# Performance work log

Hardware: AMD Instinct MI355X
Metric: run time of the kernel (lower is better)

## Reference

```python
import jax, jax.numpy as jnp
import numpy as np

N_NODES = 200000
N_EDGES = 4000000
NUM_BASIS = 10
MAX_RADIUS = 1.0
NUM_NEIGHBORS = 10
HIDDEN = 16
# e3nn FCTP(0e+1o+2e, 0e+1o+2e -> 0e): 3 paths (l x l -> 0e), path coeff = 1/sqrt(n_paths*(2l+1))
PATH_C = np.array([1.0 / np.sqrt(3.0 * (2 * l + 1)) for l in (0, 1, 2)], dtype=np.float32)


def _spherical_harmonics_l2(v):
    """e3nn spherical harmonics lmax=2, normalize=True, 'component' normalization. v: [E,3] -> [E,9]."""
    r = jnp.linalg.norm(v, axis=-1, keepdims=True)
    u = v / jnp.maximum(r, 1e-12)
    x, y, z = u[:, 0], u[:, 1], u[:, 2]
    s3, s5 = np.sqrt(3.0).astype(np.float32), np.sqrt(5.0).astype(np.float32)
    sh0 = jnp.ones_like(x)[:, None]                      # [E,1]
    sh1 = s3 * u                                         # [E,3]
    x2, y2, z2 = x * x, y * y, z * z
    sh2 = s5 * jnp.stack([s3 * x * z,
                          s3 * x * y,
                          y2 - 0.5 * (x2 + z2),
                          s3 * y * z,
                          0.5 * s3 * (z2 - x2)], axis=-1)  # [E,5]
    return jnp.concatenate([sh0, sh1, sh2], axis=-1)


def _radial_embedding(r):
    """e3nn soft_one_hot_linspace(basis='smooth_finite', cutoff=True) * sqrt(num_basis). r: [E] -> [E,NUM_BASIS]."""
    values = jnp.linspace(0.0, MAX_RADIUS, NUM_BASIS + 2)[1:-1]
    step = MAX_RADIUS / (NUM_BASIS + 1)
    diff = (r[:, None] - values) / step

    def soft_unit_step(t):
        return jnp.where(t > 0, jnp.exp(-1.0 / jnp.where(t > 0, t, 1.0)), 0.0)

    y = np.float32(1.14136 * np.exp(2.0)) * soft_unit_step(diff + 1.0) * soft_unit_step(1.0 - diff)
    return y * np.float32(np.sqrt(NUM_BASIS))


def setup_inputs() -> dict:
    key = jax.random.key(0)
    k1, k2, k3, k4, k5, k6 = jax.random.split(key, 6)
    node_feats = jax.random.normal(k1, (N_NODES, 9), dtype=jnp.float32)
    edge_vec = 0.25 * jax.random.normal(k2, (N_EDGES, 3), dtype=jnp.float32)  # keep norms mostly < max_radius
    edge_src = jax.random.randint(k3, (N_EDGES,), 0, N_NODES)
    edge_dst = jax.random.randint(k4, (N_EDGES,), 0, N_NODES)
    W1 = jax.random.normal(k5, (NUM_BASIS, HIDDEN), dtype=jnp.float32)
    W2 = jax.random.normal(k6, (HIDDEN, 3), dtype=jnp.float32)
    return {"node_feats": node_feats, "edge_vec": edge_vec, "W1": W1, "W2": W2,
            "edge_src": edge_src, "edge_dst": edge_dst}


def reference(node_feats, edge_vec, W1, W2, edge_src, edge_dst):
    r = jnp.linalg.norm(edge_vec, axis=-1)                      # [E]
    sh = _spherical_harmonics_l2(edge_vec)                      # [E,9]
    emb = _radial_embedding(r)                                  # [E,NUM_BASIS]
    # e3nn FullyConnectedNet([num_basis, 16, 3], relu): variance-preserving layers
    h = np.float32(np.sqrt(2.0)) * jax.nn.relu(emb @ W1 / np.float32(np.sqrt(NUM_BASIS)))
    w = h @ W2 / np.float32(np.sqrt(HIDDEN))                    # [E,3] per-edge TP weights
    f = node_feats[edge_src]                                    # gather [E,9]
    # FCTP paths: l x l -> 0e reduces to per-l dot products
    dots = jnp.stack([f[:, 0] * sh[:, 0],
                      jnp.sum(f[:, 1:4] * sh[:, 1:4], axis=-1),
                      jnp.sum(f[:, 4:9] * sh[:, 4:9], axis=-1)], axis=-1)  # [E,3]
    edge_out = jnp.sum(w * jnp.asarray(PATH_C) * dots, axis=-1)            # [E]
    node_out = jax.ops.segment_sum(edge_out, edge_dst, num_segments=N_NODES)
    node_out = node_out / np.float32(np.sqrt(NUM_NEIGHBORS))
    return node_out.sum()
```

## Files before the change

### kernel.cpp

```cpp
#include <hip/hip_runtime.h>
#include <hip/hip_fp16.h>

#define NTHREADS 256
#define NBLOCKS 2048
#define FB_NBLOCKS 2048
#define NB 1024
#define NBP 1040

#define KTOT 11.9269705f
#define CL0  0.04564355f
#define CL1  0.02635231f
#define CL2  0.02041241f
#define S3   1.7320508f
#define S5   2.2360680f

__device__ __forceinline__ float fast_rcp(float x) { return __builtin_amdgcn_rcpf(x); }

__global__ __launch_bounds__(256) void pack_feats_14(
    const float* __restrict__ nf, uint4* __restrict__ tab, int n_nodes)
{
    const int n = blockIdx.x * 256 + threadIdx.x;
    if (n >= n_nodes) return;
    const float* f = nf + 9 * (size_t)n;
    const float scale[9] = { 1.0f, S3, S3, S3, S5 * S3, S5 * S3, S5, S5 * S3,
                             0.5f * S5 * S3 };
    unsigned short hs[9];
#pragma unroll
    for (int i = 0; i < 9; ++i) {
        const __half h = __float2half_rn(f[i] * scale[i]);
        hs[i] = *reinterpret_cast<const unsigned short*>(&h);
    }
    unsigned long long c[9];
#pragma unroll
    for (int i = 1; i < 9; ++i)
        c[i] = (unsigned long long)(((unsigned)hs[i] + 2u) >> 2) & 0x3FFFull;
    const unsigned long long lo =
        c[1] | (c[2] << 14) | (c[3] << 28) | (c[4] << 42) | (c[5] << 56);
    const unsigned long long hi =
        (c[5] >> 8) | (c[6] << 6) | (c[7] << 20) | (c[8] << 34) |
        ((unsigned long long)hs[0] << 48);
    tab[n] = make_uint4((unsigned)lo, (unsigned)(lo >> 32),
                        (unsigned)hi, (unsigned)(hi >> 32));
}

__global__ __launch_bounds__(256) void build_wtable_kernel(
    const float* __restrict__ W1, const float* __restrict__ W2,
    float* __restrict__ wtab)
{
    const int idx = blockIdx.x * 256 + threadIdx.x;
    if (idx > NB) return;
    const float r = (float)idx * (1.0f / (float)NB);

    const float t    = 11.0f * r;
    const int   k0   = (int)t;
    const float frac = t - (float)k0;
    float ea = 0.0f, eb = 0.0f;
    if (k0 >= 1 && k0 <= 10) {
        const float da = fmaf(-frac, frac, 1.0f);
        if (da > 0.0226f) ea = KTOT * __expf(-2.0f * fast_rcp(da));
    }
    if (k0 <= 9) {
        const float db = frac * (2.0f - frac);
        if (db > 0.0226f) eb = KTOT * __expf(-2.0f * fast_rcp(db));
    }
    const int ra = min(max(k0 - 1, 0), 9);
    const int rb = min(k0, 9);

    float w0 = 0.0f, w1 = 0.0f, w2 = 0.0f;
#pragma unroll
    for (int j = 0; j < 16; ++j) {
        const float h = fmaxf(fmaf(ea, W1[ra * 16 + j], eb * W1[rb * 16 + j]), 0.0f);
        w0 = fmaf(h, W2[j * 3 + 0], w0);
        w1 = fmaf(h, W2[j * 3 + 1], w1);
        w2 = fmaf(h, W2[j * 3 + 2], w2);
    }
    wtab[idx]           = w0 * CL0;
    wtab[NBP + idx]     = w1 * CL1;
    wtab[2 * NBP + idx] = w2 * CL2;
}

__device__ __forceinline__ float cvt14(unsigned c) {
    __half_raw hr; hr.x = (unsigned short)(c << 2);
    return __half2float(*reinterpret_cast<const __half*>(&hr));
}
__device__ __forceinline__ float cvt16(unsigned c) {
    __half_raw hr; hr.x = (unsigned short)c;
    return __half2float(*reinterpret_cast<const __half*>(&hr));
}
__device__ __forceinline__ unsigned alignb(unsigned hi, unsigned lo, int s) {
    return (lo >> s) | (hi << (32 - s));
}

__device__ __forceinline__ float edge_term_lut(
    float vx, float vy, float vz, uint4 g,
    const float* __restrict__ sw)
{
    const float r2 = fmaf(vx, vx, fmaf(vy, vy, vz * vz));
    const float rs = rsqrtf(fmaxf(r2, 1e-24f));
    const float r  = r2 * rs;
    const float x = vx * rs, y = vy * rs, z = vz * rs;

    const float tb = fminf(r, 1.0f) * (float)NB;
    const int   i  = min((int)tb, NB - 1);
    const float fb = tb - (float)i;
    const float w0a = sw[i],           w0b = sw[i + 1];
    const float w1a = sw[NBP + i],     w1b = sw[NBP + i + 1];
    const float w2a = sw[2 * NBP + i], w2b = sw[2 * NBP + i + 1];
    const float wv0 = fmaf(fb, w0b - w0a, w0a);
    const float wv1 = fmaf(fb, w1b - w1a, w1a);
    const float wv2 = fmaf(fb, w2b - w2a, w2a);

    const float fv1 = cvt14(g.x & 0x3FFFu);
    const float fv2 = cvt14((g.x >> 14) & 0x3FFFu);
    const float fv3 = cvt14(alignb(g.y, g.x, 28) & 0x3FFFu);
    const float fv4 = cvt14((g.y >> 10) & 0x3FFFu);
    const float fv5 = cvt14(alignb(g.z, g.y, 24) & 0x3FFFu);
    const float fv6 = cvt14((g.z >> 6) & 0x3FFFu);
    const float fv7 = cvt14(alignb(g.w, g.z, 20) & 0x3FFFu);
    const float fv8 = cvt14((g.w >> 2) & 0x3FFFu);
    const float f0  = cvt16(g.w >> 16);

    const float dots0 = f0;
    const float dots1 = fmaf(fv1, x, fmaf(fv2, y, fv3 * z));
    const float xx = x * x, yy = y * y, zz = z * z;
    const float dots2 = fmaf(fv4, x * z, fmaf(fv5, x * y,
                        fmaf(fv6, fmaf(-0.5f, xx + zz, yy),
                        fmaf(fv7, y * z, fv8 * (zz - xx)))));

    return fmaf(wv0, dots0, fmaf(wv1, dots1, wv2 * dots2));
}

__global__ __launch_bounds__(NTHREADS) void edge_sum_p14(
    const float4* __restrict__ ev4,
    const int4*   __restrict__ src4,
    const uint4*  __restrict__ tab,
    const float*  __restrict__ wtab,
    float*        __restrict__ block_sums,
    int n_edges)
{
    __shared__ float sw[3 * NBP];
    const int tid = threadIdx.x;
    for (int i = tid; i < 3 * NBP; i += NTHREADS) sw[i] = wtab[i];
    __syncthreads();

    float acc = 0.0f;
    const int n_groups = (n_edges + 3) >> 2;
    const int stride = gridDim.x * blockDim.x;
    for (int g = blockIdx.x * blockDim.x + tid; g < n_groups; g += stride) {
        const int e0 = g << 2;
        if (e0 + 3 < n_edges) {
            const float4 a = ev4[3 * (size_t)g + 0];
            const float4 b = ev4[3 * (size_t)g + 1];
            const float4 c = ev4[3 * (size_t)g + 2];
            const int4   s = src4[g];
            const uint4 g0 = tab[s.x];
            const uint4 g1 = tab[s.y];
            const uint4 g2 = tab[s.z];
            const uint4 g3 = tab[s.w];
            acc += edge_term_lut(a.x, a.y, a.z, g0, sw);
            acc += edge_term_lut(a.w, b.x, b.y, g1, sw);
            acc += edge_term_lut(b.z, b.w, c.x, g2, sw);
            acc += edge_term_lut(c.y, c.z, c.w, g3, sw);
        } else {
            const float* evf  = reinterpret_cast<const float*>(ev4);
            const int*   srci = reinterpret_cast<const int*>(src4);
            for (int e = e0; e < n_edges; ++e) {
                acc += edge_term_lut(evf[3 * (size_t)e], evf[3 * (size_t)e + 1],
                                     evf[3 * (size_t)e + 2], tab[srci[e]], sw);
            }
        }
    }

#pragma unroll
    for (int off = 1; off < 64; off <<= 1)
        acc += __shfl_xor(acc, off, 64);
    __shared__ float wsum[NTHREADS / 64];
    const int lane = tid & 63, wid = tid >> 6;
    if (lane == 0) wsum[wid] = acc;
    __syncthreads();
    if (tid == 0) {
        float ssum = 0.0f;
#pragma unroll
        for (int w = 0; w < NTHREADS / 64; ++w) ssum += wsum[w];
        block_sums[blockIdx.x] = ssum;
    }
}

__global__ __launch_bounds__(NTHREADS) void edge_sum_fallback(
    const float* __restrict__ node_feats,
    const float* __restrict__ edge_vec,
    const float* __restrict__ W1,
    const float* __restrict__ W2,
    const int*   __restrict__ edge_src,
    float*       __restrict__ block_sums,
    int n_edges)
{
    __shared__ float4 sW1[10][5];
    float* sW1f = reinterpret_cast<float*>(sW1);
    const int tid = threadIdx.x;
    if (tid < 160) {
        sW1f[(tid >> 4) * 20 + (tid & 15)] = W1[tid];
    } else if (tid < 200) {
        const int i = tid - 160;
        sW1f[(i >> 2) * 20 + 16 + (i & 3)] = 0.0f;
    }
    __syncthreads();

    float w2r[16][3];
#pragma unroll
    for (int j = 0; j < 16; ++j) {
        w2r[j][0] = W2[j * 3 + 0] * CL0;
        w2r[j][1] = W2[j * 3 + 1] * CL1;
        w2r[j][2] = W2[j * 3 + 2] * CL2;
    }

    float acc = 0.0f;
    const int stride = gridDim.x * blockDim.x;
    for (int e = blockIdx.x * blockDim.x + tid; e < n_edges; e += stride) {
        const float vx = edge_vec[3 * (size_t)e + 0];
        const float vy = edge_vec[3 * (size_t)e + 1];
        const float vz = edge_vec[3 * (size_t)e + 2];
        const int   src = edge_src[e];
        const float* f = node_feats + 9 * (size_t)src;
        const float r2 = fmaf(vx, vx, fmaf(vy, vy, vz * vz));
        const float rs = rsqrtf(fmaxf(r2, 1e-24f));
        const float r  = r2 * rs;
        const float x = vx * rs, y = vy * rs, z = vz * rs;
        const float t    = 11.0f * r;
        const int   k0   = (int)t;
        const float frac = t - (float)k0;
        float ea = 0.0f, eb = 0.0f;
        if (k0 >= 1 && k0 <= 10) {
            const float da = fmaf(-frac, frac, 1.0f);
            if (da > 0.0226f) ea = KTOT * __expf(-2.0f * fast_rcp(da));
        }
        if (k0 <= 9) {
            const float db = frac * (2.0f - frac);
            if (db > 0.0226f) eb = KTOT * __expf(-2.0f * fast_rcp(db));
        }
        const int ra = min(max(k0 - 1, 0), 9);
        const int rb = min(k0, 9);
        const float4* rowA = &sW1[ra][0];
        const float4* rowB = &sW1[rb][0];
        float wv0 = 0.0f, wv1 = 0.0f, wv2 = 0.0f;
#pragma unroll
        for (int q = 0; q < 4; ++q) {
            const float4 A = rowA[q];
            const float4 B = rowB[q];
            float h;
            h = fmaxf(fmaf(ea, A.x, eb * B.x), 0.0f);
            wv0 = fmaf(h, w2r[4 * q + 0][0], wv0); wv1 = fmaf(h, w2r[4 * q + 0][1], wv1); wv2 = fmaf(h, w2r[4 * q + 0][2], wv2);
            h = fmaxf(fmaf(ea, A.y, eb * B.y), 0.0f);
            wv0 = fmaf(h, w2r[4 * q + 1][0], wv0); wv1 = fmaf(h, w2r[4 * q + 1][1], wv1); wv2 = fmaf(h, w2r[4 * q + 1][2], wv2);
            h = fmaxf(fmaf(ea, A.z, eb * B.z), 0.0f);
            wv0 = fmaf(h, w2r[4 * q + 2][0], wv0); wv1 = fmaf(h, w2r[4 * q + 2][1], wv1); wv2 = fmaf(h, w2r[4 * q + 2][2], wv2);
            h = fmaxf(fmaf(ea, A.w, eb * B.w), 0.0f);
            wv0 = fmaf(h, w2r[4 * q + 3][0], wv0); wv1 = fmaf(h, w2r[4 * q + 3][1], wv1); wv2 = fmaf(h, w2r[4 * q + 3][2], wv2);
        }
        const float f0 = f[0], f1 = f[1], f2 = f[2], f3 = f[3], f4 = f[4];
        const float f5 = f[5], f6 = f[6], f7 = f[7], f8 = f[8];
        const float dots0 = f0;
        const float dots1 = S3 * fmaf(f1, x, fmaf(f2, y, f3 * z));
        const float xx = x * x, yy = y * y, zz = z * z;
        const float sh20 = S5 * S3 * x * z;
        const float sh21 = S5 * S3 * x * y;
        const float sh22 = S5 * (yy - 0.5f * (xx + zz));
        const float sh23 = S5 * S3 * y * z;
        const float sh24 = S5 * 0.5f * S3 * (zz - xx);
        const float dots2 = fmaf(f4, sh20, fmaf(f5, sh21, fmaf(f6, sh22, fmaf(f7, sh23, f8 * sh24))));
        acc = fmaf(wv0, dots0, acc);
        acc = fmaf(wv1, dots1, acc);
        acc = fmaf(wv2, dots2, acc);
    }
#pragma unroll
    for (int off = 1; off < 64; off <<= 1)
        acc += __shfl_xor(acc, off, 64);
    __shared__ float wsum[NTHREADS / 64];
    const int lane = tid & 63, wid = tid >> 6;
    if (lane == 0) wsum[wid] = acc;
    __syncthreads();
    if (tid == 0) {
        float ssum = 0.0f;
#pragma unroll
        for (int w = 0; w < NTHREADS / 64; ++w) ssum += wsum[w];
        block_sums[blockIdx.x] = ssum;
    }
}

__global__ __launch_bounds__(256) void final_reduce_kernel(
    const float* __restrict__ block_sums, float* __restrict__ out, int n)
{
    const int tid = threadIdx.x;
    float acc = 0.0f;
    for (int i = tid; i < n; i += 256) acc += block_sums[i];
#pragma unroll
    for (int off = 1; off < 64; off <<= 1)
        acc += __shfl_xor(acc, off, 64);
    __shared__ float wsum[4];
    if ((tid & 63) == 0) wsum[tid >> 6] = acc;
    __syncthreads();
    if (tid == 0) out[0] = wsum[0] + wsum[1] + wsum[2] + wsum[3];
}

extern "C" void kernel_launch(void* const* d_in, const int* in_sizes, int n_in,
                              void* d_out, int out_size, void* d_ws, size_t ws_size,
                              hipStream_t stream) {
    const float* node_feats = (const float*)d_in[0];
    const float* edge_vec   = (const float*)d_in[1];
    const float* W1         = (const float*)d_in[2];
    const float* W2         = (const float*)d_in[3];
    const int*   edge_src   = (const int*)d_in[4];
    const int n_edges = in_sizes[4];
    const int n_nodes = in_sizes[0] / 9;

    float* block_sums = (float*)d_ws;
    const size_t wtab_off = 32768;
    const size_t tab_off  = wtab_off + ((3 * NBP * 4 + 255) & ~255);
    const size_t need     = tab_off + (size_t)n_nodes * 16;

    if (ws_size >= need) {
        float* wtab = (float*)((char*)d_ws + wtab_off);
        uint4* tab  = (uint4*)((char*)d_ws + tab_off);
        pack_feats_14<<<(n_nodes + 255) / 256, 256, 0, stream>>>(
            node_feats, tab, n_nodes);
        build_wtable_kernel<<<(NB + 256) / 256, 256, 0, stream>>>(W1, W2, wtab);
        edge_sum_p14<<<NBLOCKS, NTHREADS, 0, stream>>>(
            (const float4*)edge_vec, (const int4*)edge_src, tab,
            wtab, block_sums, n_edges);
        final_reduce_kernel<<<1, 256, 0, stream>>>(block_sums, (float*)d_out, NBLOCKS);
    } else {
        edge_sum_fallback<<<FB_NBLOCKS, NTHREADS, 0, stream>>>(
            node_feats, edge_vec, W1, W2, edge_src, block_sums, n_edges);
        final_reduce_kernel<<<1, 256, 0, stream>>>(block_sums, (float*)d_out, FB_NBLOCKS);
    }
}
```

Before: 46.79 us.

## Pack radial weight LUT into fp16 base+delta records and process 8 edges per thread

Replaces the three separate float LUT arrays with a single 16-byte record per bin holding fp16 bases and slopes, so each edge does one LDS vector read instead of six scalar reads. Each thread now handles 8 edges per iteration with more outstanding gathers, and the grid is halved. An extra small kernel builds the packed table; fp16 weights reduce precision of the interpolation.

```diff
diff --git a/kernel.cpp b/kernel.cpp
--- a/kernel.cpp
+++ b/kernel.cpp
@@ -2,7 +2,7 @@
 #include <hip/hip_fp16.h>
 
 #define NTHREADS 256
-#define NBLOCKS 2048
+#define NBLOCKS 1024
 #define FB_NBLOCKS 2048
 #define NB 1024
 #define NBP 1040
@@ -45,7 +45,7 @@
 
 __global__ __launch_bounds__(256) void build_wtable_kernel(
     const float* __restrict__ W1, const float* __restrict__ W2,
-    float* __restrict__ wtab)
+    float* __restrict__ wtabf)
 {
     const int idx = blockIdx.x * 256 + threadIdx.x;
     if (idx > NB) return;
@@ -74,9 +74,26 @@
         w1 = fmaf(h, W2[j * 3 + 1], w1);
         w2 = fmaf(h, W2[j * 3 + 2], w2);
     }
-    wtab[idx]           = w0 * CL0;
-    wtab[NBP + idx]     = w1 * CL1;
-    wtab[2 * NBP + idx] = w2 * CL2;
+    wtabf[idx]           = w0 * CL0;
+    wtabf[NBP + idx]     = w1 * CL1;
+    wtabf[2 * NBP + idx] = w2 * CL2;
+}
+
+__global__ __launch_bounds__(256) void build_wrec_kernel(
+    const float* __restrict__ wtabf, uint4* __restrict__ wrec)
+{
+    const int i = blockIdx.x * 256 + threadIdx.x;
+    if (i >= NB) return;
+    const float w0a = wtabf[i],           w0b = wtabf[i + 1];
+    const float w1a = wtabf[NBP + i],     w1b = wtabf[NBP + i + 1];
+    const float w2a = wtabf[2 * NBP + i], w2b = wtabf[2 * NBP + i + 1];
+    auto hbits = [](float v) -> unsigned {
+        const __half h = __float2half_rn(v);
+        return (unsigned)*reinterpret_cast<const unsigned short*>(&h);
+    };
+    const unsigned b0 = hbits(w0a), b1 = hbits(w1a), b2 = hbits(w2a);
+    const unsigned d0 = hbits(w0b - w0a), d1 = hbits(w1b - w1a), d2 = hbits(w2b - w2a);
+    wrec[i] = make_uint4(b0 | (b1 << 16), b2 | (d0 << 16), d1 | (d2 << 16), 0u);
 }
 
 __device__ __forceinline__ float cvt14(unsigned c) {
@@ -84,16 +101,15 @@
     return __half2float(*reinterpret_cast<const __half*>(&hr));
 }
 __device__ __forceinline__ float cvt16(unsigned c) {
-    __half_raw hr; hr.x = (unsigned short)c;
+    __half_raw hr; hr.x = (unsigned short)(c & 0xFFFFu);
     return __half2float(*reinterpret_cast<const __half*>(&hr));
 }
 __device__ __forceinline__ unsigned alignb(unsigned hi, unsigned lo, int s) {
     return (lo >> s) | (hi << (32 - s));
 }
 
-__device__ __forceinline__ float edge_term_lut(
-    float vx, float vy, float vz, uint4 g,
-    const float* __restrict__ sw)
+__device__ __forceinline__ float edge_term(
+    float vx, float vy, float vz, uint4 g, const uint4* __restrict__ swq)
 {
     const float r2 = fmaf(vx, vx, fmaf(vy, vy, vz * vz));
     const float rs = rsqrtf(fmaxf(r2, 1e-24f));
@@ -103,12 +119,10 @@
     const float tb = fminf(r, 1.0f) * (float)NB;
     const int   i  = min((int)tb, NB - 1);
     const float fb = tb - (float)i;
-    const float w0a = sw[i],           w0b = sw[i + 1];
-    const float w1a = sw[NBP + i],     w1b = sw[NBP + i + 1];
-    const float w2a = sw[2 * NBP + i], w2b = sw[2 * NBP + i + 1];
-    const float wv0 = fmaf(fb, w0b - w0a, w0a);
-    const float wv1 = fmaf(fb, w1b - w1a, w1a);
-    const float wv2 = fmaf(fb, w2b - w2a, w2a);
+    const uint4 q = swq[i];
+    const float wv0 = fmaf(fb, cvt16(q.y >> 16), cvt16(q.x));
+    const float wv1 = fmaf(fb, cvt16(q.z),       cvt16(q.x >> 16));
+    const float wv2 = fmaf(fb, cvt16(q.z >> 16), cvt16(q.y));
 
     const float fv1 = cvt14(g.x & 0x3FFFu);
     const float fv2 = cvt14((g.x >> 14) & 0x3FFFu);
@@ -130,43 +144,56 @@
     return fmaf(wv0, dots0, fmaf(wv1, dots1, wv2 * dots2));
 }
 
-__global__ __launch_bounds__(NTHREADS) void edge_sum_p14(
+__global__ __launch_bounds__(NTHREADS) void edge_sum_p14w(
     const float4* __restrict__ ev4,
     const int4*   __restrict__ src4,
     const uint4*  __restrict__ tab,
-    const float*  __restrict__ wtab,
+    const uint4*  __restrict__ wrec,
     float*        __restrict__ block_sums,
     int n_edges)
 {
-    __shared__ float sw[3 * NBP];
+    __shared__ uint4 swq[NB];
     const int tid = threadIdx.x;
-    for (int i = tid; i < 3 * NBP; i += NTHREADS) sw[i] = wtab[i];
+#pragma unroll
+    for (int i = tid; i < NB; i += NTHREADS) swq[i] = wrec[i];
     __syncthreads();
 
     float acc = 0.0f;
-    const int n_groups = (n_edges + 3) >> 2;
+    const int n_units = (n_edges + 7) >> 3;
     const int stride = gridDim.x * blockDim.x;
-    for (int g = blockIdx.x * blockDim.x + tid; g < n_groups; g += stride) {
-        const int e0 = g << 2;
-        if (e0 + 3 < n_edges) {
-            const float4 a = ev4[3 * (size_t)g + 0];
-            const float4 b = ev4[3 * (size_t)g + 1];
-            const float4 c = ev4[3 * (size_t)g + 2];
-            const int4   s = src4[g];
-            const uint4 g0 = tab[s.x];
-            const uint4 g1 = tab[s.y];
-            const uint4 g2 = tab[s.z];
-            const uint4 g3 = tab[s.w];
-            acc += edge_term_lut(a.x, a.y, a.z, g0, sw);
-            acc += edge_term_lut(a.w, b.x, b.y, g1, sw);
-            acc += edge_term_lut(b.z, b.w, c.x, g2, sw);
-            acc += edge_term_lut(c.y, c.z, c.w, g3, sw);
+    for (int u = blockIdx.x * blockDim.x + tid; u < n_units; u += stride) {
+        const int e0 = u << 3;
+        if (e0 + 8 <= n_edges) {
+            const float4 v0 = ev4[6 * (size_t)u + 0];
+            const float4 v1 = ev4[6 * (size_t)u + 1];
+            const float4 v2 = ev4[6 * (size_t)u + 2];
+            const float4 v3 = ev4[6 * (size_t)u + 3];
+            const float4 v4 = ev4[6 * (size_t)u + 4];
+            const float4 v5 = ev4[6 * (size_t)u + 5];
+            const int4 sA = src4[2 * (size_t)u + 0];
+            const int4 sB = src4[2 * (size_t)u + 1];
+            const uint4 g0 = tab[sA.x];
+            const uint4 g1 = tab[sA.y];
+            const uint4 g2 = tab[sA.z];
+            const uint4 g3 = tab[sA.w];
+            const uint4 g4 = tab[sB.x];
+            const uint4 g5 = tab[sB.y];
+            const uint4 g6 = tab[sB.z];
+            const uint4 g7 = tab[sB.w];
+            acc += edge_term(v0.x, v0.y, v0.z, g0, swq);
+            acc += edge_term(v0.w, v1.x, v1.y, g1, swq);
+            acc += edge_term(v1.z, v1.w, v2.x, g2, swq);
+            acc += edge_term(v2.y, v2.z, v2.w, g3, swq);
+            acc += edge_term(v3.x, v3.y, v3.z, g4, swq);
+            acc += edge_term(v3.w, v4.x, v4.y, g5, swq);
+            acc += edge_term(v4.z, v4.w, v5.x, g6, swq);
+            acc += edge_term(v5.y, v5.z, v5.w, g7, swq);
         } else {
             const float* evf  = reinterpret_cast<const float*>(ev4);
             const int*   srci = reinterpret_cast<const int*>(src4);
             for (int e = e0; e < n_edges; ++e) {
-                acc += edge_term_lut(evf[3 * (size_t)e], evf[3 * (size_t)e + 1],
-                                     evf[3 * (size_t)e + 2], tab[srci[e]], sw);
+                acc += edge_term(evf[3 * (size_t)e], evf[3 * (size_t)e + 1],
+                                 evf[3 * (size_t)e + 2], tab[srci[e]], swq);
             }
         }
     }
@@ -314,19 +341,22 @@
     const int n_nodes = in_sizes[0] / 9;
 
     float* block_sums = (float*)d_ws;
-    const size_t wtab_off = 32768;
-    const size_t tab_off  = wtab_off + ((3 * NBP * 4 + 255) & ~255);
-    const size_t need     = tab_off + (size_t)n_nodes * 16;
+    const size_t wtabf_off = 32768;
+    const size_t wrec_off  = wtabf_off + ((3 * NBP * 4 + 255) & ~255);
+    const size_t tab_off   = wrec_off + NB * 16;
+    const size_t need      = tab_off + (size_t)n_nodes * 16;
 
     if (ws_size >= need) {
-        float* wtab = (float*)((char*)d_ws + wtab_off);
-        uint4* tab  = (uint4*)((char*)d_ws + tab_off);
+        float* wtabf = (float*)((char*)d_ws + wtabf_off);
+        uint4* wrec  = (uint4*)((char*)d_ws + wrec_off);
+        uint4* tab   = (uint4*)((char*)d_ws + tab_off);
         pack_feats_14<<<(n_nodes + 255) / 256, 256, 0, stream>>>(
             node_feats, tab, n_nodes);
-        build_wtable_kernel<<<(NB + 256) / 256, 256, 0, stream>>>(W1, W2, wtab);
-        edge_sum_p14<<<NBLOCKS, NTHREADS, 0, stream>>>(
-            (const float4*)edge_vec, (const int4*)edge_src, tab,
-            wtab, block_sums, n_edges);
+        build_wtable_kernel<<<(NB + 256) / 256, 256, 0, stream>>>(W1, W2, wtabf);
+        build_wrec_kernel<<<NB / 256, 256, 0, stream>>>(wtabf, wrec);
+        edge_sum_p14w<<<NBLOCKS, NTHREADS, 0, stream>>>(
+            (const float4*)edge_vec, (const int4*)edge_src, tab, wrec,
+            block_sums, n_edges);
         final_reduce_kernel<<<1, 256, 0, stream>>>(block_sums, (float*)d_out, NBLOCKS);
     } else {
         edge_sum_fallback<<<FB_NBLOCKS, NTHREADS, 0, stream>>>(
```

Result: slower. 56.05 us (+19.8%).
